# Kernel optimization log

Hardware: AMD Instinct MI355X
Metric: run time of the kernel (lower is better)

The kernel has to match this reference:

```python
import jax, jax.numpy as jnp
import numpy as np

D_MODEL = 1024
N_HEADS = 16
HIDDEN = 256
PER_HEAD = 256
EPS = 1e-6


def setup_inputs() -> dict:
    key = jax.random.key(0)
    ks = jax.random.split(key, 6)
    B = 1024
    x = jax.random.normal(ks[0], (B, 64, D_MODEL), dtype=jnp.float32)
    # token_compress: Linear(d_model, 32, bias=False) -> weight (32, d_model)
    W_tc = jax.random.normal(ks[1], (32, D_MODEL), dtype=jnp.float32) / np.sqrt(D_MODEL)
    # global_compress: Linear(64*32, hidden) with bias, then RMSNorm(hidden)
    W_gc = jax.random.normal(ks[2], (HIDDEN, 64 * 32), dtype=jnp.float32) / np.sqrt(64 * 32)
    b_gc = jnp.zeros((HIDDEN,), dtype=jnp.float32)
    rms_scale = jnp.ones((HIDDEN,), dtype=jnp.float32)
    # per-head projections stacked: (n_heads, per_head, hidden)
    W_heads = jax.random.normal(ks[3], (N_HEADS, PER_HEAD, HIDDEN), dtype=jnp.float32) / np.sqrt(HIDDEN)
    # attn_logit_proj: Linear(per_head, 64*64, bias=False) -> (4096, per_head)
    W_logit = jax.random.normal(ks[4], (64 * 64, PER_HEAD), dtype=jnp.float32) / np.sqrt(PER_HEAD)
    return {"x": x, "W_tc": W_tc, "W_gc": W_gc, "b_gc": b_gc,
            "rms_scale": rms_scale, "W_heads": W_heads, "W_logit": W_logit}


def reference(x, W_tc, W_gc, b_gc, rms_scale, W_heads, W_logit):
    B = x.shape[0]
    # token compress: (B, 64, d_model) -> (B, 64, 32)
    compressed = jnp.einsum('bsd,kd->bsk', x, W_tc)
    flat = compressed.reshape(B, 64 * 32)
    # global compress + RMSNorm
    g = flat @ W_gc.T + b_gc                      # (B, hidden)
    rms = jnp.sqrt(jnp.mean(g * g, axis=-1, keepdims=True) + EPS)
    g = g / rms * rms_scale
    # batched per-head projection: (B, n_heads, per_head)
    head_repr = jnp.einsum('bh,nph->bnp', g, W_heads)
    # shared attn logit projection: (B, n_heads, 4096)
    logits = jnp.einsum('bnp,qp->bnq', head_repr, W_logit)
    return logits.reshape(B, N_HEADS, 64, 64)
```

## Files before the change

### kernel.cpp

```cpp
#include <hip/hip_runtime.h>


typedef unsigned short ushort_t;
typedef __attribute__((ext_vector_type(8))) short bf16x8;
typedef __attribute__((ext_vector_type(4))) float f32x4;
typedef __attribute__((ext_vector_type(4))) unsigned int u32x4;

#define MFMA16(a, b, c) __builtin_amdgcn_mfma_f32_16x16x32_bf16((a), (b), (c), 0, 0, 0)

__device__ __forceinline__ unsigned bfround(float f) {
  unsigned u = __builtin_bit_cast(unsigned, f);
  return u + 0x7fffu + ((u >> 16) & 1u);
}
__device__ __forceinline__ unsigned pack2(float lo, float hi) {
  return (bfround(lo) >> 16) | (bfround(hi) & 0xffff0000u);
}
__device__ __forceinline__ ushort_t bf1(float f) { return (ushort_t)(bfround(f) >> 16); }

__device__ __forceinline__ void gld16(const ushort_t* g, ushort_t* l) {
  __builtin_amdgcn_global_load_lds(
      (const __attribute__((address_space(1))) unsigned int*)g,
      (__attribute__((address_space(3))) unsigned int*)l, 16, 0, 0);
}

__global__ __launch_bounds__(256) void k_cvt(const float* __restrict__ Wtc,
                                             const float* __restrict__ Wgc,
                                             const float* __restrict__ Wh,
                                             const float* __restrict__ Wl,
                                             ushort_t* __restrict__ oTc,
                                             ushort_t* __restrict__ oGc,
                                             ushort_t* __restrict__ oWh,
                                             ushort_t* __restrict__ oWl) {
  size_t g = (size_t)blockIdx.x * 256 + threadIdx.x;
  const float* src; ushort_t* dst; size_t off;
  if (g < 4096)        { src = Wtc; dst = oTc; off = g; }
  else if (g < 69632)  { src = Wgc; dst = oGc; off = g - 4096; }
  else if (g < 200704) { src = Wh;  dst = oWh; off = g - 69632; }
  else                 { src = Wl;  dst = oWl; off = g - 200704; }
  float4 f0 = ((const float4*)src)[off * 2];
  float4 f1 = ((const float4*)src)[off * 2 + 1];
  u32x4 p;
  p.x = pack2(f0.x, f0.y); p.y = pack2(f0.z, f0.w);
  p.z = pack2(f1.x, f1.y); p.w = pack2(f1.z, f1.w);
  ((u32x4*)dst)[off] = p;
}

__global__ __launch_bounds__(256) void k_tok(const float* __restrict__ x,
                                             const ushort_t* __restrict__ WtcBf,
                                             ushort_t* __restrict__ flatBf) {
  __shared__ ushort_t lb[32][264];
  const int t = threadIdx.x;
  const int w = t >> 6, l = t & 63, col16 = l & 15, quad = l >> 4;
  const float* arow = x + (size_t)blockIdx.x * 65536 + (size_t)(w * 16 + col16) * 1024;
  f32x4 acc0 = {0.f, 0.f, 0.f, 0.f}, acc1 = {0.f, 0.f, 0.f, 0.f};

  for (int ko = 0; ko < 1024; ko += 256) {
    float4 af[16];
#pragma unroll
    for (int s = 0; s < 8; ++s) {
      af[2 * s]     = *(const float4*)(arow + ko + s * 32 + quad * 8);
      af[2 * s + 1] = *(const float4*)(arow + ko + s * 32 + quad * 8 + 4);
    }
    __syncthreads();
    {
      int r = t >> 3, c0 = (t & 7) * 32;
      const ushort_t* src = WtcBf + (size_t)r * 1024 + ko + c0;
#pragma unroll
      for (int c = 0; c < 4; ++c)
        *(bf16x8*)&lb[r][c0 + c * 8] = *(const bf16x8*)(src + c * 8);
    }
    __syncthreads();
#pragma unroll
    for (int s = 0; s < 8; ++s) {
      u32x4 p;
      p.x = pack2(af[2 * s].x, af[2 * s].y);
      p.y = pack2(af[2 * s].z, af[2 * s].w);
      p.z = pack2(af[2 * s + 1].x, af[2 * s + 1].y);
      p.w = pack2(af[2 * s + 1].z, af[2 * s + 1].w);
      bf16x8 a = __builtin_bit_cast(bf16x8, p);
      bf16x8 b0 = *(const bf16x8*)&lb[col16][s * 32 + quad * 8];
      bf16x8 b1 = *(const bf16x8*)&lb[16 + col16][s * 32 + quad * 8];
      acc0 = MFMA16(a, b0, acc0);
      acc1 = MFMA16(a, b1, acc1);
    }
  }
  ushort_t* ob = flatBf + (size_t)blockIdx.x * 2048;
#pragma unroll
  for (int r = 0; r < 4; ++r) {
    int m = w * 16 + quad * 4 + r;
    ob[m * 32 + col16]      = bf1(acc0[r]);
    ob[m * 32 + 16 + col16] = bf1(acc1[r]);
  }
}

__global__ __launch_bounds__(256) void k_gc_part(const ushort_t* __restrict__ Abf,
                                                 const ushort_t* __restrict__ Bbf,
                                                 float* __restrict__ Hpart) {
  __shared__ ushort_t la[16][40];
  __shared__ ushort_t lb[256][40];
  const int t = threadIdx.x;
  const int w = t >> 6, l = t & 63, col16 = l & 15, quad = l >> 4;
  const int b0 = blockIdx.x * 16;
  const int k0 = blockIdx.y * 512;
  f32x4 acc[4];
#pragma unroll
  for (int j = 0; j < 4; ++j) acc[j] = (f32x4){0.f, 0.f, 0.f, 0.f};

  for (int kk = 0; kk < 512; kk += 32) {
    __syncthreads();
    if (t < 128) {
      int r = t >> 3, c0 = (t & 7) * 4;
      *(ushort4*)&la[r][c0] =
          *(const ushort4*)(Abf + (size_t)(b0 + r) * 2048 + k0 + kk + c0);
    }
    {
      const ushort_t* src = Bbf + (size_t)t * 2048 + k0 + kk;
#pragma unroll
      for (int c = 0; c < 4; ++c)
        *(bf16x8*)&lb[t][c * 8] = *(const bf16x8*)(src + c * 8);
    }
    __syncthreads();
    bf16x8 af = *(const bf16x8*)&la[col16][quad * 8];
#pragma unroll
    for (int j = 0; j < 4; ++j) {
      bf16x8 bf = *(const bf16x8*)&lb[w * 64 + j * 16 + col16][quad * 8];
      acc[j] = MFMA16(af, bf, acc[j]);
    }
  }
  float* o = Hpart + (size_t)blockIdx.y * 262144;
#pragma unroll
  for (int j = 0; j < 4; ++j)
#pragma unroll
    for (int r = 0; r < 4; ++r)
      o[(size_t)(b0 + quad * 4 + r) * 256 + w * 64 + j * 16 + col16] = acc[j][r];
}

__global__ __launch_bounds__(256) void k_gc_red(const float* __restrict__ Hpart,
                                                const float* __restrict__ bias,
                                                const float* __restrict__ rscale,
                                                ushort_t* __restrict__ gBf) {
  __shared__ float lred[16][17];
  __shared__ float linv[16];
  const int t = threadIdx.x;
  const int row = t >> 4, seg = t & 15;
  const size_t base = (size_t)(blockIdx.x * 16 + row) * 256 + seg * 16;
  float v[16];
#pragma unroll
  for (int k = 0; k < 4; ++k) {
    float4 s0 = *(const float4*)(Hpart + base + k * 4);
    float4 s1 = *(const float4*)(Hpart + 262144 + base + k * 4);
    float4 s2 = *(const float4*)(Hpart + 524288 + base + k * 4);
    float4 s3 = *(const float4*)(Hpart + 786432 + base + k * 4);
    float4 bi = *(const float4*)(bias + seg * 16 + k * 4);
    v[k * 4 + 0] = s0.x + s1.x + s2.x + s3.x + bi.x;
    v[k * 4 + 1] = s0.y + s1.y + s2.y + s3.y + bi.y;
    v[k * 4 + 2] = s0.z + s1.z + s2.z + s3.z + bi.z;
    v[k * 4 + 3] = s0.w + s1.w + s2.w + s3.w + bi.w;
  }
  float ss = 0.f;
#pragma unroll
  for (int k = 0; k < 16; ++k) ss += v[k] * v[k];
  lred[row][seg] = ss;
  __syncthreads();
  if (t < 16) {
    float s = 0.f;
#pragma unroll
    for (int k = 0; k < 16; ++k) s += lred[t][k];
    linv[t] = 1.0f / sqrtf(s * (1.0f / 256.0f) + 1e-6f);
  }
  __syncthreads();
  float iv = linv[row];
  float rs[16];
#pragma unroll
  for (int k = 0; k < 4; ++k)
    *(float4*)&rs[k * 4] = *(const float4*)(rscale + seg * 16 + k * 4);
  u32x4 p0, p1;
  p0.x = pack2(v[0] * iv * rs[0],  v[1] * iv * rs[1]);
  p0.y = pack2(v[2] * iv * rs[2],  v[3] * iv * rs[3]);
  p0.z = pack2(v[4] * iv * rs[4],  v[5] * iv * rs[5]);
  p0.w = pack2(v[6] * iv * rs[6],  v[7] * iv * rs[7]);
  p1.x = pack2(v[8] * iv * rs[8],  v[9] * iv * rs[9]);
  p1.y = pack2(v[10] * iv * rs[10], v[11] * iv * rs[11]);
  p1.z = pack2(v[12] * iv * rs[12], v[13] * iv * rs[13]);
  p1.w = pack2(v[14] * iv * rs[14], v[15] * iv * rs[15]);
  *(u32x4*)(gBf + base) = p0;
  *(u32x4*)(gBf + base + 8) = p1;
}

template <bool OBF>
__global__ __launch_bounds__(256) void k_gemm(const ushort_t* __restrict__ A,
                                              const ushort_t* __restrict__ Bw,
                                              float* __restrict__ Cf,
                                              ushort_t* __restrict__ Cb) {
  __shared__ ushort_t la[128 * 64];
  __shared__ ushort_t lb[128 * 64];
  const int t = threadIdx.x;
  const int w = t >> 6, l = t & 63, col16 = l & 15, quad = l >> 4;
  const int wm = w >> 1, wn = w & 1;
  const size_t am0 = (size_t)blockIdx.y * 128;
  const size_t bn0 = (size_t)blockIdx.x * 128;

  f32x4 acc[4][4];
#pragma unroll
  for (int i = 0; i < 4; ++i)
#pragma unroll
    for (int j = 0; j < 4; ++j) acc[i][j] = (f32x4){0.f, 0.f, 0.f, 0.f};

  for (int kk = 0; kk < 256; kk += 64) {
    __syncthreads();
#pragma unroll
    for (int i = 0; i < 4; ++i) {
      int L = i * 256 + t;
      int r = L >> 3;
      int cs = (L & 7) ^ (r & 7);
      ushort_t* ldst_a = la + (size_t)((i * 256 + (w << 6)) << 3);
      ushort_t* ldst_b = lb + (size_t)((i * 256 + (w << 6)) << 3);
      gld16(A + (am0 + r) * 256 + kk + cs * 8, ldst_a);
      gld16(Bw + (bn0 + r) * 256 + kk + cs * 8, ldst_b);
    }
    __syncthreads();
#pragma unroll
    for (int k2 = 0; k2 < 64; k2 += 32) {
      const int cg = (k2 >> 3) + quad;
      bf16x8 af[4], bf[4];
#pragma unroll
      for (int i = 0; i < 4; ++i) {
        int R = wm * 64 + i * 16 + col16;
        af[i] = *(const bf16x8*)(la + (size_t)((R * 8 + (cg ^ (R & 7))) << 3));
      }
#pragma unroll
      for (int j = 0; j < 4; ++j) {
        int R = wn * 64 + j * 16 + col16;
        bf[j] = *(const bf16x8*)(lb + (size_t)((R * 8 + (cg ^ (R & 7))) << 3));
      }
#pragma unroll
      for (int i = 0; i < 4; ++i)
#pragma unroll
        for (int j = 0; j < 4; ++j)
          acc[i][j] = MFMA16(af[i], bf[j], acc[i][j]);
    }
  }
#pragma unroll
  for (int i = 0; i < 4; ++i)
#pragma unroll
    for (int j = 0; j < 4; ++j)
#pragma unroll
      for (int r = 0; r < 4; ++r) {
        size_t row = am0 + wm * 64 + i * 16 + quad * 4 + r;
        size_t c = bn0 + wn * 64 + j * 16 + col16;
        if (OBF) Cb[row * 4096 + c] = bf1(acc[i][j][r]);
        else     Cf[row * 4096 + c] = acc[i][j][r];
      }
}

extern "C" void kernel_launch(void* const* d_in, const int* in_sizes, int n_in,
                              void* d_out, int out_size, void* d_ws, size_t ws_size,
                              hipStream_t stream) {
  const float* x   = (const float*)d_in[0];
  const float* Wtc = (const float*)d_in[1];
  const float* Wgc = (const float*)d_in[2];
  const float* bgc = (const float*)d_in[3];
  const float* rsc = (const float*)d_in[4];
  const float* Wh  = (const float*)d_in[5];
  const float* Wl  = (const float*)d_in[6];
  float* out = (float*)d_out;

  char* ws = (char*)d_ws;
  ushort_t* oTc    = (ushort_t*)(ws);
  ushort_t* oGc    = (ushort_t*)(ws + 65536);
  ushort_t* oWh    = (ushort_t*)(ws + 1114112);
  ushort_t* oWl    = (ushort_t*)(ws + 3211264);
  ushort_t* flatBf = (ushort_t*)(ws + 5308416);
  ushort_t* gBf    = (ushort_t*)(ws + 9502720);
  ushort_t* HBf    = (ushort_t*)(ws + 10027008);
  float*    Hpart  = (float*)(ws + 18415616);

  k_cvt<<<1296, 256, 0, stream>>>(Wtc, Wgc, Wh, Wl, oTc, oGc, oWh, oWl);
  k_tok<<<1024, 256, 0, stream>>>(x, oTc, flatBf);
  k_gc_part<<<dim3(64, 4), 256, 0, stream>>>(flatBf, oGc, Hpart);
  k_gc_red<<<64, 256, 0, stream>>>(Hpart, bgc, rsc, gBf);
  k_gemm<true><<<dim3(32, 8), 256, 0, stream>>>(gBf, oWh, nullptr, HBf);
  k_gemm<false><<<dim3(32, 128), 256, 0, stream>>>(HBf, oWl, out, nullptr);
}
```

Before: 523.6 us.

## Swap MFMA operands for vectorized stores, double-buffer GEMM loads, remap blocks

Swaps the A/B operands of every MFMA so each lane holds four consecutive output columns. Stores then become 8/16-byte vector writes instead of scalar writes, which matters most for the large fp32 logits GEMM output. The GEMM also moves to a 32-wide K step with double-buffered LDS staging, so the next tile's loads overlap the current MFMAs. It also uses a 1D grid with an XCD-aware block-index remap for better L2 locality. The trade-off is more barriers per K (8 iterations instead of 4) and a different LDS swizzle.

```diff
diff --git a/kernel.cpp b/kernel.cpp
--- a/kernel.cpp
+++ b/kernel.cpp
@@ -5,6 +5,7 @@
 typedef __attribute__((ext_vector_type(8))) short bf16x8;
 typedef __attribute__((ext_vector_type(4))) float f32x4;
 typedef __attribute__((ext_vector_type(4))) unsigned int u32x4;
+typedef __attribute__((ext_vector_type(2))) unsigned int u32x2;
 
 #define MFMA16(a, b, c) __builtin_amdgcn_mfma_f32_16x16x32_bf16((a), (b), (c), 0, 0, 0)
 
@@ -15,7 +16,6 @@
 __device__ __forceinline__ unsigned pack2(float lo, float hi) {
   return (bfround(lo) >> 16) | (bfround(hi) & 0xffff0000u);
 }
-__device__ __forceinline__ ushort_t bf1(float f) { return (ushort_t)(bfround(f) >> 16); }
 
 __device__ __forceinline__ void gld16(const ushort_t* g, ushort_t* l) {
   __builtin_amdgcn_global_load_lds(
@@ -80,17 +80,17 @@
       bf16x8 a = __builtin_bit_cast(bf16x8, p);
       bf16x8 b0 = *(const bf16x8*)&lb[col16][s * 32 + quad * 8];
       bf16x8 b1 = *(const bf16x8*)&lb[16 + col16][s * 32 + quad * 8];
-      acc0 = MFMA16(a, b0, acc0);
-      acc1 = MFMA16(a, b1, acc1);
+      acc0 = MFMA16(b0, a, acc0);
+      acc1 = MFMA16(b1, a, acc1);
     }
   }
   ushort_t* ob = flatBf + (size_t)blockIdx.x * 2048;
-#pragma unroll
-  for (int r = 0; r < 4; ++r) {
-    int m = w * 16 + quad * 4 + r;
-    ob[m * 32 + col16]      = bf1(acc0[r]);
-    ob[m * 32 + 16 + col16] = bf1(acc1[r]);
-  }
+  const int m = w * 16 + col16;
+  u32x2 v0, v1;
+  v0.x = pack2(acc0[0], acc0[1]); v0.y = pack2(acc0[2], acc0[3]);
+  v1.x = pack2(acc1[0], acc1[1]); v1.y = pack2(acc1[2], acc1[3]);
+  *(u32x2*)&ob[m * 32 + quad * 4] = v0;
+  *(u32x2*)&ob[m * 32 + 16 + quad * 4] = v1;
 }
 
 __global__ __launch_bounds__(256) void k_gc_part(const ushort_t* __restrict__ Abf,
@@ -123,16 +123,14 @@
     bf16x8 af = *(const bf16x8*)&la[col16][quad * 8];
 #pragma unroll
     for (int j = 0; j < 4; ++j) {
-      bf16x8 bf = *(const bf16x8*)&lb[w * 64 + j * 16 + col16][quad * 8];
-      acc[j] = MFMA16(af, bf, acc[j]);
+      bf16x8 bfj = *(const bf16x8*)&lb[w * 64 + j * 16 + col16][quad * 8];
+      acc[j] = MFMA16(bfj, af, acc[j]);
     }
   }
   float* o = Hpart + (size_t)blockIdx.y * 262144;
 #pragma unroll
   for (int j = 0; j < 4; ++j)
-#pragma unroll
-    for (int r = 0; r < 4; ++r)
-      o[(size_t)(b0 + quad * 4 + r) * 256 + w * 64 + j * 16 + col16] = acc[j][r];
+    *(f32x4*)&o[(size_t)(b0 + col16) * 256 + w * 64 + j * 16 + quad * 4] = acc[j];
 }
 
 __global__ __launch_bounds__(256) void k_gc_red(const float* __restrict__ Hpart,
@@ -192,13 +190,15 @@
                                               const ushort_t* __restrict__ Bw,
                                               float* __restrict__ Cf,
                                               ushort_t* __restrict__ Cb) {
-  __shared__ ushort_t la[128 * 64];
-  __shared__ ushort_t lb[128 * 64];
+  __shared__ ushort_t la[2][4096];
+  __shared__ ushort_t lb[2][4096];
   const int t = threadIdx.x;
   const int w = t >> 6, l = t & 63, col16 = l & 15, quad = l >> 4;
   const int wm = w >> 1, wn = w & 1;
-  const size_t am0 = (size_t)blockIdx.y * 128;
-  const size_t bn0 = (size_t)blockIdx.x * 128;
+  const int id = blockIdx.x;
+  const int id2 = (id & 7) * ((int)gridDim.x >> 3) + (id >> 3);
+  const size_t am0 = (size_t)(id2 >> 5) * 128;
+  const size_t bn0 = (size_t)(id2 & 31) * 128;
 
   f32x4 acc[4][4];
 #pragma unroll
@@ -206,51 +206,59 @@
 #pragma unroll
     for (int j = 0; j < 4; ++j) acc[i][j] = (f32x4){0.f, 0.f, 0.f, 0.f};
 
-  for (int kk = 0; kk < 256; kk += 64) {
-    __syncthreads();
+  auto STAGE = [&](int buf, int kk) {
+#pragma unroll
+    for (int i = 0; i < 2; ++i) {
+      int L = i * 256 + t;
+      int r = L >> 2;
+      int cs = (L & 3) ^ (r & 3);
+      ushort_t* da = &la[buf][(size_t)(i * 256 + (w << 6)) * 8];
+      ushort_t* db = &lb[buf][(size_t)(i * 256 + (w << 6)) * 8];
+      gld16(A + (am0 + r) * 256 + kk + cs * 8, da);
+      gld16(Bw + (bn0 + r) * 256 + kk + cs * 8, db);
+    }
+  };
+
+  STAGE(0, 0);
+  __syncthreads();
+#pragma unroll
+  for (int tix = 0; tix < 8; ++tix) {
+    const int buf = tix & 1;
+    if (tix < 7) STAGE(buf ^ 1, (tix + 1) * 32);
+    bf16x8 af[4], bfv[4];
 #pragma unroll
     for (int i = 0; i < 4; ++i) {
-      int L = i * 256 + t;
-      int r = L >> 3;
-      int cs = (L & 7) ^ (r & 7);
-      ushort_t* ldst_a = la + (size_t)((i * 256 + (w << 6)) << 3);
-      ushort_t* ldst_b = lb + (size_t)((i * 256 + (w << 6)) << 3);
-      gld16(A + (am0 + r) * 256 + kk + cs * 8, ldst_a);
-      gld16(Bw + (bn0 + r) * 256 + kk + cs * 8, ldst_b);
-    }
-    __syncthreads();
-#pragma unroll
-    for (int k2 = 0; k2 < 64; k2 += 32) {
-      const int cg = (k2 >> 3) + quad;
-      bf16x8 af[4], bf[4];
-#pragma unroll
-      for (int i = 0; i < 4; ++i) {
-        int R = wm * 64 + i * 16 + col16;
-        af[i] = *(const bf16x8*)(la + (size_t)((R * 8 + (cg ^ (R & 7))) << 3));
+      int R = wm * 64 + i * 16 + col16;
+      af[i] = *(const bf16x8*)&la[buf][(size_t)((R << 2) + (quad ^ (R & 3))) * 8];
+    }
+#pragma unroll
+    for (int j = 0; j < 4; ++j) {
+      int R = wn * 64 + j * 16 + col16;
+      bfv[j] = *(const bf16x8*)&lb[buf][(size_t)((R << 2) + (quad ^ (R & 3))) * 8];
+    }
+#pragma unroll
+    for (int i = 0; i < 4; ++i)
+#pragma unroll
+      for (int j = 0; j < 4; ++j)
+        acc[i][j] = MFMA16(bfv[j], af[i], acc[i][j]);
+    __syncthreads();
+  }
+
+#pragma unroll
+  for (int i = 0; i < 4; ++i)
+#pragma unroll
+    for (int j = 0; j < 4; ++j) {
+      size_t row = am0 + wm * 64 + i * 16 + col16;
+      size_t cc = bn0 + wn * 64 + j * 16 + quad * 4;
+      if (OBF) {
+        u32x2 v;
+        v.x = pack2(acc[i][j][0], acc[i][j][1]);
+        v.y = pack2(acc[i][j][2], acc[i][j][3]);
+        *(u32x2*)&Cb[row * 4096 + cc] = v;
+      } else {
+        *(f32x4*)&Cf[row * 4096 + cc] = acc[i][j];
       }
-#pragma unroll
-      for (int j = 0; j < 4; ++j) {
-        int R = wn * 64 + j * 16 + col16;
-        bf[j] = *(const bf16x8*)(lb + (size_t)((R * 8 + (cg ^ (R & 7))) << 3));
-      }
-#pragma unroll
-      for (int i = 0; i < 4; ++i)
-#pragma unroll
-        for (int j = 0; j < 4; ++j)
-          acc[i][j] = MFMA16(af[i], bf[j], acc[i][j]);
-    }
-  }
-#pragma unroll
-  for (int i = 0; i < 4; ++i)
-#pragma unroll
-    for (int j = 0; j < 4; ++j)
-#pragma unroll
-      for (int r = 0; r < 4; ++r) {
-        size_t row = am0 + wm * 64 + i * 16 + quad * 4 + r;
-        size_t c = bn0 + wn * 64 + j * 16 + col16;
-        if (OBF) Cb[row * 4096 + c] = bf1(acc[i][j][r]);
-        else     Cf[row * 4096 + c] = acc[i][j][r];
-      }
+    }
 }
 
 extern "C" void kernel_launch(void* const* d_in, const int* in_sizes, int n_in,
@@ -279,6 +287,6 @@
   k_tok<<<1024, 256, 0, stream>>>(x, oTc, flatBf);
   k_gc_part<<<dim3(64, 4), 256, 0, stream>>>(flatBf, oGc, Hpart);
   k_gc_red<<<64, 256, 0, stream>>>(Hpart, bgc, rsc, gBf);
-  k_gemm<true><<<dim3(32, 8), 256, 0, stream>>>(gBf, oWh, nullptr, HBf);
-  k_gemm<false><<<dim3(32, 128), 256, 0, stream>>>(HBf, oWl, out, nullptr);
-}
+  k_gemm<true><<<256, 256, 0, stream>>>(gBf, oWh, nullptr, HBf);
+  k_gemm<false><<<4096, 256, 0, stream>>>(HBf, oWl, out, nullptr);
+}
```

New measurement: 524.0 us. Within noise of the previous version (+0.1%).
